# Optimization experiments

Hardware: AMD Instinct MI355X
Metric: run time of the kernel (lower is better)

The kernel has to match this reference:

```python
import jax, jax.numpy as jnp
import numpy as np

B, T, HOR, N = 32, 12, 12, 883
D = 10      # embed_dim == time_dim
HID = 64    # rnn_units
OUT = 1     # output_dim
K = 2       # cheb_k: supports [I, A]


def _pdg2(x, e1, e2, E, Wp, bp):
    # x:[B,N,Ci]  e1,e2:[B,N,D]  E:[N,D]  Wp:[D,K,Ci,Co]  bp:[D,Co]
    nv1 = jnp.tanh(E[None] * e1)                      # [B,N,D]
    nv2 = jnp.tanh(E[None] * e2)
    A = jax.nn.softmax(jax.nn.relu(jnp.einsum('bnd,bmd->bnm', nv1, nv2)), axis=-1)
    xg = jnp.stack([x, jnp.einsum('bnm,bmc->bnc', A, x)], axis=2)   # [B,N,K,Ci]
    W = jnp.einsum('bnd,dkio->bnkio', nv1, Wp)        # node/time-adaptive weights
    b = jnp.einsum('bnd,do->bno', nv1, bp)
    return jnp.einsum('bnki,bnkio->bno', xg, W) + b


def _cell(x, h, e1, e2, E, gW, gb, uW, ub):
    xs = jnp.concatenate([x, h], axis=-1)
    zr = jax.nn.sigmoid(_pdg2(xs, e1, e2, E, gW, gb))
    z, r = jnp.split(zr, 2, axis=-1)
    cand = jnp.concatenate([x, z * h], axis=-1)
    hc = jnp.tanh(_pdg2(cand, e1, e2, E, uW, ub))
    return r * h + (1.0 - r) * hc


def setup_inputs() -> dict:
    key = jax.random.key(0)
    ks = jax.random.split(key, 20)
    s = 0.1
    inp = {
        'src_vals': jax.random.normal(ks[0], (B, T, N, 1), jnp.float32),
        'node_emb': s * jax.random.normal(ks[1], (N, D), jnp.float32),
        'tid_emb1': s * jax.random.normal(ks[2], (288, D), jnp.float32),
        'tid_emb2': s * jax.random.normal(ks[3], (288, D), jnp.float32),
        'diw_emb1': s * jax.random.normal(ks[4], (7, D), jnp.float32),
        'diw_emb2': s * jax.random.normal(ks[5], (7, D), jnp.float32),
        'enc_gate_W': s * jax.random.normal(ks[6], (D, K, 1 + HID, 2 * HID), jnp.float32),
        'enc_gate_b': s * jax.random.normal(ks[7], (D, 2 * HID), jnp.float32),
        'enc_upd_W': s * jax.random.normal(ks[8], (D, K, 1 + HID, HID), jnp.float32),
        'enc_upd_b': s * jax.random.normal(ks[9], (D, HID), jnp.float32),
        'dec_gate_W': s * jax.random.normal(ks[10], (D, K, OUT + HID, 2 * HID), jnp.float32),
        'dec_gate_b': s * jax.random.normal(ks[11], (D, 2 * HID), jnp.float32),
        'dec_upd_W': s * jax.random.normal(ks[12], (D, K, OUT + HID, HID), jnp.float32),
        'dec_upd_b': s * jax.random.normal(ks[13], (D, HID), jnp.float32),
        'proj_W': s * jax.random.normal(ks[14], (OUT, HID), jnp.float32),
        'proj_b': jnp.zeros((OUT,), jnp.float32),
        'src_tid': jax.random.randint(ks[15], (B, T, N), 0, 288, jnp.int32),
        'src_diw': jax.random.randint(ks[16], (B, T, N), 0, 7, jnp.int32),
        'tgt_tid': jax.random.randint(ks[17], (B, HOR, N), 0, 288, jnp.int32),
        'tgt_diw': jax.random.randint(ks[18], (B, HOR, N), 0, 7, jnp.int32),
    }
    return inp


def reference(src_vals, node_emb, tid_emb1, tid_emb2, diw_emb1, diw_emb2,
              enc_gate_W, enc_gate_b, enc_upd_W, enc_upd_b,
              dec_gate_W, dec_gate_b, dec_upd_W, dec_upd_b,
              proj_W, proj_b, src_tid, src_diw, tgt_tid, tgt_diw):
    tm = lambda a: jnp.swapaxes(a, 0, 1)   # batch-major -> time-major
    # periodic embeddings (use_week=True -> elementwise product)
    e1_en = tid_emb1[src_tid] * diw_emb1[src_diw]   # [B,T,N,D]
    e2_en = tid_emb2[src_tid] * diw_emb2[src_diw]
    e1_de = tid_emb1[tgt_tid] * diw_emb1[tgt_diw]   # [B,HOR,N,D]
    e2_de = tid_emb2[tgt_tid] * diw_emb2[tgt_diw]

    h0 = jnp.zeros((src_vals.shape[0], node_emb.shape[0], HID), src_vals.dtype)

    def enc_step(h, inp):
        x, e1, e2 = inp
        h = _cell(x, h, e1, e2, node_emb, enc_gate_W, enc_gate_b, enc_upd_W, enc_upd_b)
        return h, None

    h, _ = jax.lax.scan(enc_step, h0, (tm(src_vals), tm(e1_en), tm(e2_en)))

    go0 = jnp.zeros((src_vals.shape[0], node_emb.shape[0], OUT), src_vals.dtype)

    def dec_step(carry, inp):
        h, go = carry
        e1, e2 = inp
        h = _cell(go, h, e1, e2, node_emb, dec_gate_W, dec_gate_b, dec_upd_W, dec_upd_b)
        go = h @ proj_W.T + proj_b
        return (h, go), go

    _, outs = jax.lax.scan(dec_step, (h, go0), (tm(e1_de), tm(e2_de)))
    return jnp.swapaxes(outs, 0, 1)   # [B,HOR,N,OUT]
```

## Files before the change

### kernel.cpp

```cpp
#include <hip/hip_runtime.h>

#define BB 32
#define TSRC 12
#define HORZ 12
#define NN 883
#define DD 10
#define HH 64
#define BN (BB*NN)
#define BNP 28288
#define KF 5
#define NT 14
#define NST (TSRC+HORZ)

typedef __attribute__((ext_vector_type(8))) short short8;
typedef __attribute__((ext_vector_type(4))) float f32x4;

static __device__ __forceinline__ float sigmf(float x) { return 1.f/(1.f + __expf(-x)); }
static __device__ __forceinline__ float tanh_fast(float x) {
  float e = __expf(2.f*x);
  return (e - 1.f) / (e + 1.f);
}
static __device__ __forceinline__ unsigned int bf_hi(float f) {
  unsigned int u = __float_as_uint(f);
  return (u + 0x7fffu + ((u >> 16) & 1u)) >> 16;
}
static __device__ __forceinline__ float bf_f(unsigned int h) {
  return __uint_as_float(h << 16);
}
static __device__ __forceinline__ void lds_load16(const void* g, void* l) {
  __builtin_amdgcn_global_load_lds(
      (const __attribute__((address_space(1))) void*)g,
      (__attribute__((address_space(3))) void*)l, 16, 0, 0);
}

static __device__ __forceinline__ void swz_block(int& b, int& rt) {
  int lin = blockIdx.x + blockIdx.y*NT;
  int c = lin & 7, q = lin >> 3;
  b = c + ((q/NT) << 3);
  rt = q - (q/NT)*NT;
}

static __device__ __forceinline__ void xs_store(unsigned short* chunk, int c, int mm2, float v) {
  int p0 = (c*128 + (mm2 ^ ((c & 7) << 4))) >> 1;
  unsigned int hi = bf_hi(v);
  chunk[p0] = (unsigned short)hi;
  chunk[p0 + 4096] = (unsigned short)bf_hi(v - bf_f(hi));
}

__global__ __launch_bounds__(256) void prep_all(
    const float* __restrict__ tidE1, const float* __restrict__ tidE2,
    const float* __restrict__ diwE1, const float* __restrict__ diwE2,
    const float* __restrict__ nodeE,
    const int* __restrict__ stid, const int* __restrict__ sdiw,
    const int* __restrict__ ttid, const int* __restrict__ tdiw,
    const float* __restrict__ xsrc,
    float* __restrict__ nv1A, float* __restrict__ nv2A,
    unsigned short* __restrict__ XsH, unsigned short* __restrict__ XsZ)
{
  int i = blockIdx.x*256 + threadIdx.x;
  if (i >= BN) return;
  int st = blockIdx.y;
  int b = i / NN, n = i - b*NN;
  const int* tix = (st < TSRC) ? stid : ttid;
  const int* dix = (st < TSRC) ? sdiw : tdiw;
  int t = (st < TSRC) ? st : st - TSRC;
  int gi = (b*TSRC + t)*NN + n;
  int ti = tix[gi]*DD, di = dix[gi]*DD;
  int nE = n*DD;
  float* nv1T = nv1A + (size_t)st*DD*BNP;
  float* nv2T = nv2A + (size_t)st*DD*BNP;
#pragma unroll
  for (int d = 0; d < DD; ++d) {
    float E = nodeE[nE+d];
    nv1T[d*BNP+i] = tanh_fast(E * (tidE1[ti+d] * diwE1[di+d]));
    nv2T[d*BNP+i] = tanh_fast(E * (tidE2[ti+d] * diwE2[di+d]));
  }
  if (st == 0) {
    float xv = xsrc[gi];
    size_t cb = ((size_t)(b*NT + (n >> 6)))*8192;
    int mm = n & 63;
    unsigned int hi = bf_hi(xv);
    unsigned short los = (unsigned short)bf_hi(xv - bf_f(hi));
    XsH[cb + mm] = (unsigned short)hi; XsH[cb + 4096 + mm] = los;
    XsZ[cb + mm] = (unsigned short)hi; XsZ[cb + 4096 + mm] = los;
  }
}

__global__ __launch_bounds__(256) void wsplit_kernel(
    const float* __restrict__ W, const float* __restrict__ bias,
    int NO, unsigned short* __restrict__ Wf)
{
  int i = blockIdx.x*256 + threadIdx.x;
  int total = DD*2*KF*4*NO*8;
  if (i >= total) return;
  int j = i & 7; int r = i >> 3;
  int o = r % NO; r /= NO;
  int quad = r & 3; r >>= 2;
  int kf = r % KF; r /= KF;
  int hl = r & 1; int d = r >> 1;
  int kk = kf*32 + quad*8 + j;
  float v = 0.f;
  if (kk <= 64)       v = W[(size_t)(d*130 + kk)*NO + o];
  else if (kk == 65)  v = bias[d*NO + o];
  else if (kk <= 130) v = W[(size_t)(d*130 + kk - 1)*NO + o];
  unsigned int hi = bf_hi(v);
  Wf[i] = (hl == 0) ? (unsigned short)hi : (unsigned short)bf_hi(v - bf_f(hi));
}


__global__ __launch_bounds__(256,3) void attn_gate(
    const float* __restrict__ nv1T, const float* __restrict__ nv2T,
    const unsigned short* __restrict__ Xs,
    const float* __restrict__ h,
    const unsigned short* __restrict__ Wf,
    float* __restrict__ rbuf,
    unsigned short* __restrict__ XsZ, float* __restrict__ zh63)
{
  __shared__ float nv1s[DD][64];
  __shared__ float linv[64];
  __shared__ alignas(16) unsigned char U[46080];
  unsigned short* XT = (unsigned short*)U;
  unsigned short* PT = (unsigned short*)(U + 16384);
  float* nv2s = (float*)(U + 34816);
  float* xcolb = (float*)(U + 39936);
  int b, rt;
  swz_block(b, rt);
  int r0 = rt*64;
  int tid = threadIdx.x;
  int rg = tid >> 4, cg = tid & 15;
  int base = b*NN;
  int lane = tid & 63, lm = lane & 15, quad = lane >> 4;
  int w = tid >> 6, mp = w >> 1, np = w & 1;
  const unsigned short* XsB = Xs + (size_t)b*NT*8192;

  for (int idx = tid; idx < DD*64; idx += 256) {
    int d = idx >> 6, r = idx & 63;
    nv1s[d][r] = (r0 + r < NN) ? nv1T[d*BNP + base + r0 + r] : 0.f;
  }

  int4 xt[4];
  float nvr[3]; float xcr;
  {
    const int4* s0 = (const int4*)XsB;
#pragma unroll
    for (int i = 0; i < 4; ++i) xt[i] = s0[w*64 + lane + i*256];
#pragma unroll
    for (int i = 0; i < 3; ++i) {
      int idx = tid + i*256; float v = 0.f;
      if (idx < DD*64) { int d = idx>>6, m = idx&63; v = (m < NN) ? nv2T[d*BNP + base + m] : 0.f; }
      nvr[i] = v;
    }
    xcr = (tid < 64 && tid < NN) ? h[(size_t)63*BNP + base + tid] : 0.f;
#pragma unroll
    for (int i = 0; i < 4; ++i)
      *(int4*)((char*)XT + w*1024 + lane*16 + i*4096) = xt[i];
#pragma unroll
    for (int i = 0; i < 3; ++i) {
      int idx = tid + i*256;
      if (idx < DD*64) nv2s[idx] = nvr[i];
    }
    if (tid < 64) xcolb[tid] = xcr;
  }
  __syncthreads();

  f32x4 accv[2][2] = {};
  float acclp[4] = {}, acc5p[4] = {};

  for (int tI = 0; tI < NT; ++tI) {
    int cur = tI & 1, nxt = cur ^ 1;
    int m0 = tI*64, m0n = m0 + 64;
    bool hasn = tI < NT-1;
    if (hasn) {
      const int4* src = (const int4*)(XsB + (size_t)(tI+1)*8192);
#pragma unroll
      for (int i = 0; i < 4; ++i) xt[i] = src[w*64 + lane + i*256];
#pragma unroll
      for (int i = 0; i < 3; ++i) {
        int idx = tid + i*256; float v = 0.f;
        if (idx < DD*64) { int d = idx>>6, m = idx&63; v = (m0n + m < NN) ? nv2T[d*BNP + base + m0n + m] : 0.f; }
        nvr[i] = v;
      }
      xcr = (tid < 64 && m0n + tid < NN) ? h[(size_t)63*BNP + base + m0n + tid] : 0.f;
    }
    float s[4][4] = {};
#pragma unroll
    for (int d = 0; d < DD; ++d) {
      float4 a4 = *(const float4*)&nv1s[d][rg*4];
      float4 c4 = *(const float4*)&nv2s[cur*(DD*64) + d*64 + cg*4];
      const float* ap = (const float*)&a4;
      const float* cp = (const float*)&c4;
#pragma unroll
      for (int j = 0; j < 4; ++j)
#pragma unroll
        for (int jj = 0; jj < 4; ++jj)
          s[j][jj] += ap[j]*cp[jj];
    }
    int mvlim = NN - m0;
    float ev[4][4];
#pragma unroll
    for (int jj = 0; jj < 4; ++jj) {
      int m = cg*4 + jj;
      float xm = xcolb[cur*64 + m];
      bool okm = m < mvlim;
#pragma unroll
      for (int j = 0; j < 4; ++j) {
        float e = okm ? __expf(fmaxf(s[j][jj], 0.f)) : 0.f;
        ev[j][jj] = e;
        acclp[j] += e;
        acc5p[j] = fmaf(e, xm, acc5p[j]);
      }
    }
    {
      unsigned int* P1 = (unsigned int*)PT;
      unsigned int* P2 = (unsigned int*)(PT + 64*72);
#pragma unroll
      for (int j = 0; j < 4; ++j) {
        int r = rg*4 + j;
        unsigned int h0 = bf_hi(ev[j][0]), h1 = bf_hi(ev[j][1]), h2 = bf_hi(ev[j][2]), h3 = bf_hi(ev[j][3]);
        unsigned int l0 = bf_hi(ev[j][0]-bf_f(h0)), l1 = bf_hi(ev[j][1]-bf_f(h1));
        unsigned int l2 = bf_hi(ev[j][2]-bf_f(h2)), l3 = bf_hi(ev[j][3]-bf_f(h3));
        int dw = r*36 + cg*2;
        P1[dw] = h0 | (h1 << 16); P1[dw+1] = h2 | (h3 << 16);
        P2[dw] = l0 | (l1 << 16); P2[dw+1] = l2 | (l3 << 16);
      }
    }
    __syncthreads();
    {
      short8 Aa[2][2], Ab[2][2], Ba[2][2], Bb[2][2];
#pragma unroll
      for (int mt = 0; mt < 2; ++mt) {
        int r = mp*32 + mt*16 + lm;
#pragma unroll
        for (int kf = 0; kf < 2; ++kf) {
          Aa[mt][kf] = *(const short8*)&PT[r*72 + quad*8 + kf*32];
          Ab[mt][kf] = *(const short8*)&PT[64*72 + r*72 + quad*8 + kf*32];
        }
      }
#pragma unroll
      for (int ntl = 0; ntl < 2; ++ntl) {
        int c = np*32 + ntl*16 + lm;
        int swz = (c & 7) << 4;
        int cb0 = c*128 + quad*16;
#pragma unroll
        for (int kf = 0; kf < 2; ++kf) {
          int a = (cb0 + kf*64) ^ swz;
          Ba[ntl][kf] = *(const short8*)((const char*)XT + a);
          Bb[ntl][kf] = *(const short8*)((const char*)XT + a + 8192);
        }
      }
#pragma unroll
      for (int kf = 0; kf < 2; ++kf)
#pragma unroll
        for (int mt = 0; mt < 2; ++mt)
#pragma unroll
          for (int ntl = 0; ntl < 2; ++ntl) {
            accv[mt][ntl] = __builtin_amdgcn_mfma_f32_16x16x32_bf16(Aa[mt][kf], Ba[ntl][kf], accv[mt][ntl], 0,0,0);
            accv[mt][ntl] = __builtin_amdgcn_mfma_f32_16x16x32_bf16(Aa[mt][kf], Bb[ntl][kf], accv[mt][ntl], 0,0,0);
            accv[mt][ntl] = __builtin_amdgcn_mfma_f32_16x16x32_bf16(Ab[mt][kf], Ba[ntl][kf], accv[mt][ntl], 0,0,0);
          }
    }
    if (hasn) {
#pragma unroll
      for (int i = 0; i < 3; ++i) {
        int idx = tid + i*256;
        if (idx < DD*64) nv2s[nxt*(DD*64) + idx] = nvr[i];
      }
      if (tid < 64) xcolb[nxt*64 + tid] = xcr;
    }
    __syncthreads();
    if (hasn) {
#pragma unroll
      for (int i = 0; i < 4; ++i)
        *(int4*)((char*)XT + w*1024 + lane*16 + i*4096) = xt[i];
    }
  }
  int mrow_x = tid >> 2, ksub = tid & 3;
  int gmx = base + r0 + mrow_x;
  const unsigned short* chk_in = Xs + (size_t)(b*NT + rt)*8192;
  int mm2x = mrow_x*2;
  unsigned int pjh[9], pjl[9];
  {
    float r63v = h[(size_t)63*BNP + gmx];
    unsigned int h63 = bf_hi(r63v);
    unsigned int l63 = bf_hi(r63v - bf_f(h63));
#pragma unroll
    for (int i = 0; i < 9; ++i) {
      int kk = ksub*2 + 8*i;
      unsigned int h0 = 0, l0 = 0, h1 = 0, l1 = 0;
      if (kk <= 63) {
        int idx = (kk*128 + (mm2x ^ ((kk & 7) << 4))) >> 1;
        h0 = chk_in[idx]; l0 = chk_in[idx + 4096];
      } else if (kk == 64) { h0 = h63; l0 = l63; }
      int k1 = kk + 1;
      if (kk <= 62) {
        int idx1 = (k1*128 + (mm2x ^ ((k1 & 7) << 4))) >> 1;
        h1 = chk_in[idx1]; l1 = chk_in[idx1 + 4096];
      } else if (k1 == 65) { h1 = 0x3F80u; l1 = 0u; }
      pjh[i] = h0 | (h1 << 16);
      pjl[i] = l0 | (l1 << 16);
    }
  }
#pragma unroll
  for (int off = 1; off <= 8; off <<= 1)
#pragma unroll
    for (int j = 0; j < 4; ++j) {
      acclp[j] += __shfl_xor(acclp[j], off, 64);
      acc5p[j] += __shfl_xor(acc5p[j], off, 64);
    }
  __syncthreads();
  {
    unsigned int* Z = (unsigned int*)(U + 36864);
    for (int idx = tid; idx < 2304; idx += 256) Z[idx] = 0;
  }
  __syncthreads();
  unsigned short* XA = (unsigned short*)U;
  if (cg == 0) {
#pragma unroll
    for (int j = 0; j < 4; ++j) {
      float li = 1.f / acclp[j];
      int r = rg*4 + j;
      linv[r] = li;
      float v = acc5p[j]*li;
      unsigned int hi = bf_hi(v);
      XA[(4*64 + r)*72 + 2] = (unsigned short)hi;
      XA[(4*64 + r)*72 + 32 + 2] = (unsigned short)bf_hi(v - bf_f(hi));
    }
  }
  __syncthreads();
#pragma unroll
  for (int mt = 0; mt < 2; ++mt) {
    int rbase = mp*32 + mt*16 + quad*4;
    float4 lv = *(const float4*)&linv[rbase];
    const float* lvp = (const float*)&lv;
#pragma unroll
    for (int ntl = 0; ntl < 2; ++ntl) {
      int c = np*32 + ntl*16 + lm;
      int kk = 66 + c;
      int kf = kk >> 5, kkl = kk & 31;
#pragma unroll
      for (int r4 = 0; r4 < 4; ++r4) {
        float v = accv[mt][ntl][r4] * lvp[r4];
        unsigned int hi = bf_hi(v);
        int p = (kf*64 + rbase + r4)*72 + kkl;
        XA[p] = (unsigned short)hi;
        XA[p + 32] = (unsigned short)bf_hi(v - bf_f(hi));
      }
    }
  }
  {
    unsigned int* X1 = (unsigned int*)U;
#pragma unroll
    for (int i = 0; i < 9; ++i) {
      int kk = ksub*2 + 8*i;
      if (kk > 64) continue;
      int kf = kk >> 5, kkl = kk & 31;
      int dw = (kf*64 + mrow_x)*36 + (kkl >> 1);
      X1[dw] = pjh[i];
      X1[dw + 16] = pjl[i];
    }
  }
  __syncthreads();
  short8 A1[2][KF], A2[2][KF];
#pragma unroll
  for (int mt = 0; mt < 2; ++mt) {
    int mrow = mp*32 + mt*16 + lm;
#pragma unroll
    for (int kf = 0; kf < KF; ++kf) {
      A1[mt][kf] = *(const short8*)&XA[(kf*64 + mrow)*72 + quad*8];
      A2[mt][kf] = *(const short8*)&XA[(kf*64 + mrow)*72 + 32 + quad*8];
    }
  }
  __syncthreads();
  unsigned char* bufA = U;
  unsigned char* bufB = U + 20480;
  const int colb = np*32 + lm;
#pragma unroll 1
  for (int co = 0; co < 2; ++co) {
    int co0 = co*64;
    {
      const unsigned short* src = Wf + ((size_t)(w*5)*128 + co0)*8 + lane*8;
#pragma unroll
      for (int i = 0; i < 5; ++i)
        lds_load16(src + (size_t)i*128*8, bufA + (w*5+i)*1024);
    }
    f32x4 accO[2][2] = {};
#pragma unroll 1
    for (int d = 0; d < DD; ++d) {
      f32x4 td[2][2] = {};
      __syncthreads();
      {
        const unsigned short* src = Wf + ((size_t)((d*2+1)*20 + w*5)*128 + co0)*8 + lane*8;
#pragma unroll
        for (int i = 0; i < 5; ++i)
          lds_load16(src + (size_t)i*128*8, bufB + (w*5+i)*1024);
      }
#pragma unroll
      for (int kf = 0; kf < KF; ++kf) {
        int cb = ((kf*4 + quad)*64 + colb)*16;
#pragma unroll
        for (int ntl = 0; ntl < 2; ++ntl) {
          short8 Bh = *(const short8*)(bufA + cb + ntl*256);
          td[0][ntl] = __builtin_amdgcn_mfma_f32_16x16x32_bf16(A1[0][kf], Bh, td[0][ntl], 0,0,0);
          td[0][ntl] = __builtin_amdgcn_mfma_f32_16x16x32_bf16(A2[0][kf], Bh, td[0][ntl], 0,0,0);
          td[1][ntl] = __builtin_amdgcn_mfma_f32_16x16x32_bf16(A1[1][kf], Bh, td[1][ntl], 0,0,0);
          td[1][ntl] = __builtin_amdgcn_mfma_f32_16x16x32_bf16(A2[1][kf], Bh, td[1][ntl], 0,0,0);
        }
      }
      __syncthreads();
      if (d < DD-1) {
        const unsigned short* src = Wf + ((size_t)((d+1)*2*20 + w*5)*128 + co0)*8 + lane*8;
#pragma unroll
        for (int i = 0; i < 5; ++i)
          lds_load16(src + (size_t)i*128*8, bufA + (w*5+i)*1024);
      }
#pragma unroll
      for (int kf = 0; kf < KF; ++kf) {
        int cb = ((kf*4 + quad)*64 + colb)*16;
#pragma unroll
        for (int ntl = 0; ntl < 2; ++ntl) {
          short8 Bl = *(const short8*)(bufB + cb + ntl*256);
          td[0][ntl] = __builtin_amdgcn_mfma_f32_16x16x32_bf16(A1[0][kf], Bl, td[0][ntl], 0,0,0);
          td[1][ntl] = __builtin_amdgcn_mfma_f32_16x16x32_bf16(A1[1][kf], Bl, td[1][ntl], 0,0,0);
        }
      }
#pragma unroll
      for (int mt = 0; mt < 2; ++mt) {
        float4 nv4 = *(const float4*)&nv1s[d][mp*32 + mt*16 + quad*4];
        const float* nvp = (const float*)&nv4;
#pragma unroll
        for (int ntl = 0; ntl < 2; ++ntl)
#pragma unroll
          for (int r = 0; r < 4; ++r)
            accO[mt][ntl][r] += nvp[r] * td[mt][ntl][r];
      }
    }
    float* CT = (float*)U;
    __syncthreads();
#pragma unroll
    for (int mt = 0; mt < 2; ++mt)
#pragma unroll
      for (int ntl = 0; ntl < 2; ++ntl)
#pragma unroll
        for (int r = 0; r < 4; ++r)
          CT[(mp*32 + mt*16 + quad*4 + r)*67 + np*32 + ntl*16 + lm] = accO[mt][ntl][r];
    __syncthreads();
    {
      int mm = tid & 63, og = tid >> 6;
      int n = r0 + mm;
      int gm = base + n;
      bool okn = n < NN;
      if (co == 0) {
        unsigned short* chk = XsZ + ((size_t)(b*NT + rt))*8192;
        int mm2 = mm*2;
        for (int j = 0; j < 16; ++j) {
          int o = og*16 + j;
          float z = sigmf(CT[mm*67 + o]);
          float zhv = z * h[(size_t)o*BNP + gm];
          if (okn) {
            if (o < 63) xs_store(chk, o + 1, mm2, zhv);
            else zh63[gm] = zhv;
          }
        }
      } else {
        for (int j = 0; j < 16; ++j) {
          int o = og*16 + j;
          if (okn) rbuf[(size_t)o*BNP + gm] = sigmf(CT[mm*67 + o]);
        }
      }
    }
    __syncthreads();
  }
}

__global__ __launch_bounds__(256,3) void attn_upd(
    const float* __restrict__ nv1T, const float* __restrict__ nv2T,
    const unsigned short* __restrict__ Xs,
    const float* __restrict__ zh63,
    float* __restrict__ hstate,
    const unsigned short* __restrict__ Wf,
    const float* __restrict__ rbuf,
    int dec, const float* __restrict__ pW, const float* __restrict__ pb,
    float* __restrict__ go, float* __restrict__ dout,
    unsigned short* __restrict__ XsH, int t,
    const float* __restrict__ xsrc, int xnmode, int xnt,
    unsigned short* __restrict__ XsZm)
{
  __shared__ float nv1s[DD][64];
  __shared__ float linv[64];
  __shared__ alignas(16) unsigned char U[46080];
  unsigned short* XT = (unsigned short*)U;
  unsigned short* PT = (unsigned short*)(U + 16384);
  float* nv2s = (float*)(U + 34816);
  float* xcolb = (float*)(U + 39936);
  int b, rt;
  swz_block(b, rt);
  int r0 = rt*64;
  int tid = threadIdx.x;
  int rg = tid >> 4, cg = tid & 15;
  int base = b*NN;
  int lane = tid & 63, lm = lane & 15, quad = lane >> 4;
  int w = tid >> 6, mp = w >> 1, np = w & 1;
  const unsigned short* XsB = Xs + (size_t)b*NT*8192;

  for (int idx = tid; idx < DD*64; idx += 256) {
    int d = idx >> 6, r = idx & 63;
    nv1s[d][r] = (r0 + r < NN) ? nv1T[d*BNP + base + r0 + r] : 0.f;
  }

  int4 xt[4];
  float nvr[3]; float xcr;
  {
    const int4* s0 = (const int4*)XsB;
#pragma unroll
    for (int i = 0; i < 4; ++i) xt[i] = s0[w*64 + lane + i*256];
#pragma unroll
    for (int i = 0; i < 3; ++i) {
      int idx = tid + i*256; float v = 0.f;
      if (idx < DD*64) { int d = idx>>6, m = idx&63; v = (m < NN) ? nv2T[d*BNP + base + m] : 0.f; }
      nvr[i] = v;
    }
    xcr = (tid < 64 && tid < NN) ? zh63[base + tid] : 0.f;
#pragma unroll
    for (int i = 0; i < 4; ++i)
      *(int4*)((char*)XT + w*1024 + lane*16 + i*4096) = xt[i];
#pragma unroll
    for (int i = 0; i < 3; ++i) {
      int idx = tid + i*256;
      if (idx < DD*64) nv2s[idx] = nvr[i];
    }
    if (tid < 64) xcolb[tid] = xcr;
  }
  __syncthreads();

  f32x4 accv[2][2] = {};
  float acclp[4] = {}, acc5p[4] = {};

  for (int tI = 0; tI < NT; ++tI) {
    int cur = tI & 1, nxt = cur ^ 1;
    int m0 = tI*64, m0n = m0 + 64;
    bool hasn = tI < NT-1;
    if (hasn) {
      const int4* src = (const int4*)(XsB + (size_t)(tI+1)*8192);
#pragma unroll
      for (int i = 0; i < 4; ++i) xt[i] = src[w*64 + lane + i*256];
#pragma unroll
      for (int i = 0; i < 3; ++i) {
        int idx = tid + i*256; float v = 0.f;
        if (idx < DD*64) { int d = idx>>6, m = idx&63; v = (m0n + m < NN) ? nv2T[d*BNP + base + m0n + m] : 0.f; }
        nvr[i] = v;
      }
      xcr = (tid < 64 && m0n + tid < NN) ? zh63[base + m0n + tid] : 0.f;
    }
    float s[4][4] = {};
#pragma unroll
    for (int d = 0; d < DD; ++d) {
      float4 a4 = *(const float4*)&nv1s[d][rg*4];
      float4 c4 = *(const float4*)&nv2s[cur*(DD*64) + d*64 + cg*4];
      const float* ap = (const float*)&a4;
      const float* cp = (const float*)&c4;
#pragma unroll
      for (int j = 0; j < 4; ++j)
#pragma unroll
        for (int jj = 0; jj < 4; ++jj)
          s[j][jj] += ap[j]*cp[jj];
    }
    int mvlim = NN - m0;
    float ev[4][4];
#pragma unroll
    for (int jj = 0; jj < 4; ++jj) {
      int m = cg*4 + jj;
      float xm = xcolb[cur*64 + m];
      bool okm = m < mvlim;
#pragma unroll
      for (int j = 0; j < 4; ++j) {
        float e = okm ? __expf(fmaxf(s[j][jj], 0.f)) : 0.f;
        ev[j][jj] = e;
        acclp[j] += e;
        acc5p[j] = fmaf(e, xm, acc5p[j]);
      }
    }
    {
      unsigned int* P1 = (unsigned int*)PT;
      unsigned int* P2 = (unsigned int*)(PT + 64*72);
#pragma unroll
      for (int j = 0; j < 4; ++j) {
        int r = rg*4 + j;
        unsigned int h0 = bf_hi(ev[j][0]), h1 = bf_hi(ev[j][1]), h2 = bf_hi(ev[j][2]), h3 = bf_hi(ev[j][3]);
        unsigned int l0 = bf_hi(ev[j][0]-bf_f(h0)), l1 = bf_hi(ev[j][1]-bf_f(h1));
        unsigned int l2 = bf_hi(ev[j][2]-bf_f(h2)), l3 = bf_hi(ev[j][3]-bf_f(h3));
        int dw = r*36 + cg*2;
        P1[dw] = h0 | (h1 << 16); P1[dw+1] = h2 | (h3 << 16);
        P2[dw] = l0 | (l1 << 16); P2[dw+1] = l2 | (l3 << 16);
      }
    }
    __syncthreads();
    {
      short8 Aa[2][2], Ab[2][2], Ba[2][2], Bb[2][2];
#pragma unroll
      for (int mt = 0; mt < 2; ++mt) {
        int r = mp*32 + mt*16 + lm;
#pragma unroll
        for (int kf = 0; kf < 2; ++kf) {
          Aa[mt][kf] = *(const short8*)&PT[r*72 + quad*8 + kf*32];
          Ab[mt][kf] = *(const short8*)&PT[64*72 + r*72 + quad*8 + kf*32];
        }
      }
#pragma unroll
      for (int ntl = 0; ntl < 2; ++ntl) {
        int c = np*32 + ntl*16 + lm;
        int swz = (c & 7) << 4;
        int cb0 = c*128 + quad*16;
#pragma unroll
        for (int kf = 0; kf < 2; ++kf) {
          int a = (cb0 + kf*64) ^ swz;
          Ba[ntl][kf] = *(const short8*)((const char*)XT + a);
          Bb[ntl][kf] = *(const short8*)((const char*)XT + a + 8192);
        }
      }
#pragma unroll
      for (int kf = 0; kf < 2; ++kf)
#pragma unroll
        for (int mt = 0; mt < 2; ++mt)
#pragma unroll
          for (int ntl = 0; ntl < 2; ++ntl) {
            accv[mt][ntl] = __builtin_amdgcn_mfma_f32_16x16x32_bf16(Aa[mt][kf], Ba[ntl][kf], accv[mt][ntl], 0,0,0);
            accv[mt][ntl] = __builtin_amdgcn_mfma_f32_16x16x32_bf16(Aa[mt][kf], Bb[ntl][kf], accv[mt][ntl], 0,0,0);
            accv[mt][ntl] = __builtin_amdgcn_mfma_f32_16x16x32_bf16(Ab[mt][kf], Ba[ntl][kf], accv[mt][ntl], 0,0,0);
          }
    }
    if (hasn) {
#pragma unroll
      for (int i = 0; i < 3; ++i) {
        int idx = tid + i*256;
        if (idx < DD*64) nv2s[nxt*(DD*64) + idx] = nvr[i];
      }
      if (tid < 64) xcolb[nxt*64 + tid] = xcr;
    }
    __syncthreads();
    if (hasn) {
#pragma unroll
      for (int i = 0; i < 4; ++i)
        *(int4*)((char*)XT + w*1024 + lane*16 + i*4096) = xt[i];
    }
  }
  int mrow_x = tid >> 2, ksub = tid & 3;
  int gmx = base + r0 + mrow_x;
  const unsigned short* chk_in = Xs + (size_t)(b*NT + rt)*8192;
  int mm2x = mrow_x*2;
  unsigned int pjh[9], pjl[9];
  {
    float r63v = zh63[gmx];
    unsigned int h63 = bf_hi(r63v);
    unsigned int l63 = bf_hi(r63v - bf_f(h63));
#pragma unroll
    for (int i = 0; i < 9; ++i) {
      int kk = ksub*2 + 8*i;
      unsigned int h0 = 0, l0 = 0, h1 = 0, l1 = 0;
      if (kk <= 63) {
        int idx = (kk*128 + (mm2x ^ ((kk & 7) << 4))) >> 1;
        h0 = chk_in[idx]; l0 = chk_in[idx + 4096];
      } else if (kk == 64) { h0 = h63; l0 = l63; }
      int k1 = kk + 1;
      if (kk <= 62) {
        int idx1 = (k1*128 + (mm2x ^ ((k1 & 7) << 4))) >> 1;
        h1 = chk_in[idx1]; l1 = chk_in[idx1 + 4096];
      } else if (k1 == 65) { h1 = 0x3F80u; l1 = 0u; }
      pjh[i] = h0 | (h1 << 16);
      pjl[i] = l0 | (l1 << 16);
    }
  }
#pragma unroll
  for (int off = 1; off <= 8; off <<= 1)
#pragma unroll
    for (int j = 0; j < 4; ++j) {
      acclp[j] += __shfl_xor(acclp[j], off, 64);
      acc5p[j] += __shfl_xor(acc5p[j], off, 64);
    }
  __syncthreads();
  {
    unsigned int* Z = (unsigned int*)(U + 36864);
    for (int idx = tid; idx < 2304; idx += 256) Z[idx] = 0;
  }
  __syncthreads();
  unsigned short* XA = (unsigned short*)U;
  if (cg == 0) {
#pragma unroll
    for (int j = 0; j < 4; ++j) {
      float li = 1.f / acclp[j];
      int r = rg*4 + j;
      linv[r] = li;
      float v = acc5p[j]*li;
      unsigned int hi = bf_hi(v);
      XA[(4*64 + r)*72 + 2] = (unsigned short)hi;
      XA[(4*64 + r)*72 + 32 + 2] = (unsigned short)bf_hi(v - bf_f(hi));
    }
  }
  __syncthreads();
#pragma unroll
  for (int mt = 0; mt < 2; ++mt) {
    int rbase = mp*32 + mt*16 + quad*4;
    float4 lv = *(const float4*)&linv[rbase];
    const float* lvp = (const float*)&lv;
#pragma unroll
    for (int ntl = 0; ntl < 2; ++ntl) {
      int c = np*32 + ntl*16 + lm;
      int kk = 66 + c;
      int kf = kk >> 5, kkl = kk & 31;
#pragma unroll
      for (int r4 = 0; r4 < 4; ++r4) {
        float v = accv[mt][ntl][r4] * lvp[r4];
        unsigned int hi = bf_hi(v);
        int p = (kf*64 + rbase + r4)*72 + kkl;
        XA[p] = (unsigned short)hi;
        XA[p + 32] = (unsigned short)bf_hi(v - bf_f(hi));
      }
    }
  }
  {
    unsigned int* X1 = (unsigned int*)U;
#pragma unroll
    for (int i = 0; i < 9; ++i) {
      int kk = ksub*2 + 8*i;
      if (kk > 64) continue;
      int kf = kk >> 5, kkl = kk & 31;
      int dw = (kf*64 + mrow_x)*36 + (kkl >> 1);
      X1[dw] = pjh[i];
      X1[dw + 16] = pjl[i];
    }
  }
  __syncthreads();
  short8 A1[2][KF], A2[2][KF];
#pragma unroll
  for (int mt = 0; mt < 2; ++mt) {
    int mrow = mp*32 + mt*16 + lm;
#pragma unroll
    for (int kf = 0; kf < KF; ++kf) {
      A1[mt][kf] = *(const short8*)&XA[(kf*64 + mrow)*72 + quad*8];
      A2[mt][kf] = *(const short8*)&XA[(kf*64 + mrow)*72 + 32 + quad*8];
    }
  }
  __syncthreads();
  unsigned char* bufA = U;
  unsigned char* bufB = U + 20480;
  const int colb = np*32 + lm;
  {
    const unsigned short* src = Wf + (size_t)(w*5)*64*8 + lane*8;
#pragma unroll
    for (int i = 0; i < 5; ++i)
      lds_load16(src + (size_t)i*64*8, bufA + (w*5+i)*1024);
  }
  f32x4 accO[2][2] = {};
#pragma unroll 1
  for (int d = 0; d < DD; ++d) {
    f32x4 td[2][2] = {};
    __syncthreads();
    {
      const unsigned short* src = Wf + (size_t)((d*2+1)*20 + w*5)*64*8 + lane*8;
#pragma unroll
      for (int i = 0; i < 5; ++i)
        lds_load16(src + (size_t)i*64*8, bufB + (w*5+i)*1024);
    }
#pragma unroll
    for (int kf = 0; kf < KF; ++kf) {
      int cb = ((kf*4 + quad)*64 + colb)*16;
#pragma unroll
      for (int ntl = 0; ntl < 2; ++ntl) {
        short8 Bh = *(const short8*)(bufA + cb + ntl*256);
        td[0][ntl] = __builtin_amdgcn_mfma_f32_16x16x32_bf16(A1[0][kf], Bh, td[0][ntl], 0,0,0);
        td[0][ntl] = __builtin_amdgcn_mfma_f32_16x16x32_bf16(A2[0][kf], Bh, td[0][ntl], 0,0,0);
        td[1][ntl] = __builtin_amdgcn_mfma_f32_16x16x32_bf16(A1[1][kf], Bh, td[1][ntl], 0,0,0);
        td[1][ntl] = __builtin_amdgcn_mfma_f32_16x16x32_bf16(A2[1][kf], Bh, td[1][ntl], 0,0,0);
      }
    }
    __syncthreads();
    if (d < DD-1) {
      const unsigned short* src = Wf + (size_t)((d+1)*2*20 + w*5)*64*8 + lane*8;
#pragma unroll
      for (int i = 0; i < 5; ++i)
        lds_load16(src + (size_t)i*64*8, bufA + (w*5+i)*1024);
    }
#pragma unroll
    for (int kf = 0; kf < KF; ++kf) {
      int cb = ((kf*4 + quad)*64 + colb)*16;
#pragma unroll
      for (int ntl = 0; ntl < 2; ++ntl) {
        short8 Bl = *(const short8*)(bufB + cb + ntl*256);
        td[0][ntl] = __builtin_amdgcn_mfma_f32_16x16x32_bf16(A1[0][kf], Bl, td[0][ntl], 0,0,0);
        td[1][ntl] = __builtin_amdgcn_mfma_f32_16x16x32_bf16(A1[1][kf], Bl, td[1][ntl], 0,0,0);
      }
    }
#pragma unroll
    for (int mt = 0; mt < 2; ++mt) {
      float4 nv4 = *(const float4*)&nv1s[d][mp*32 + mt*16 + quad*4];
      const float* nvp = (const float*)&nv4;
#pragma unroll
      for (int ntl = 0; ntl < 2; ++ntl)
#pragma unroll
        for (int r = 0; r < 4; ++r)
          accO[mt][ntl][r] += nvp[r] * td[mt][ntl][r];
    }
  }
  float* CT = (float*)U;
  __syncthreads();
#pragma unroll
  for (int mt = 0; mt < 2; ++mt)
#pragma unroll
    for (int ntl = 0; ntl < 2; ++ntl)
#pragma unroll
      for (int r = 0; r < 4; ++r)
        CT[(mp*32 + mt*16 + quad*4 + r)*67 + np*32 + ntl*16 + lm] = accO[mt][ntl][r];
  __syncthreads();
  {
    int mm = tid & 63, og = tid >> 6;
    int n = r0 + mm;
    int gm = base + n;
    bool okn = n < NN;
    unsigned short* chk = XsH + ((size_t)(b*NT + rt))*8192;
    int mm2 = mm*2;
    float pp = 0.f;
    float sval = 0.f;
    for (int j = 0; j < 16; ++j) {
      int o = og*16 + j;
      float hc = tanhf(CT[mm*67 + o]);
      float r = rbuf[(size_t)o*BNP + gm];
      float hv = hstate[(size_t)o*BNP + gm];
      float hn = r*hv + (1.f - r)*hc;
      if (okn) {
        hstate[(size_t)o*BNP + gm] = hn;
        if (o < 63) xs_store(chk, o + 1, mm2, hn);
      }
      if (dec) pp = fmaf(hn, pW[o], pp);
    }
    if (dec) {
      float* PS = CT + 64*67;
      __syncthreads();
      PS[mm*4 + og] = pp;
      __syncthreads();
      if (tid < 64) {
        int n2 = r0 + tid;
        if (n2 < NN) {
          float s = pb[0] + PS[tid*4] + PS[tid*4+1] + PS[tid*4+2] + PS[tid*4+3];
          go[base + n2] = s;
          dout[(b*HORZ + t)*NN + n2] = s;
          sval = s;
        }
      }
    }
    if (xnmode) {
      if (tid < 64) {
        int n2 = r0 + tid;
        if (n2 < NN) {
          float xn;
          if (xnmode == 1)      xn = xsrc[(b*TSRC + xnt)*NN + n2];
          else if (xnmode == 2) xn = 0.f;
          else                  xn = sval;
          unsigned int hix = bf_hi(xn);
          unsigned short lox = (unsigned short)bf_hi(xn - bf_f(hix));
          unsigned short* cH = XsH + ((size_t)(b*NT + rt))*8192;
          unsigned short* cZ = XsZm + ((size_t)(b*NT + rt))*8192;
          cH[tid] = (unsigned short)hix; cH[4096 + tid] = lox;
          cZ[tid] = (unsigned short)hix; cZ[4096 + tid] = lox;
        }
      }
    }
  }
}

extern "C" void kernel_launch(void* const* d_in, const int* in_sizes, int n_in,
                              void* d_out, int out_size, void* d_ws, size_t ws_size,
                              hipStream_t stream) {
  (void)in_sizes; (void)n_in; (void)out_size; (void)ws_size;
  const float* src_vals = (const float*)d_in[0];
  const float* node_emb = (const float*)d_in[1];
  const float* tid1 = (const float*)d_in[2];
  const float* tid2 = (const float*)d_in[3];
  const float* diw1 = (const float*)d_in[4];
  const float* diw2 = (const float*)d_in[5];
  const float* egW = (const float*)d_in[6];
  const float* egb = (const float*)d_in[7];
  const float* euW = (const float*)d_in[8];
  const float* eub = (const float*)d_in[9];
  const float* dgW = (const float*)d_in[10];
  const float* dgb = (const float*)d_in[11];
  const float* duW = (const float*)d_in[12];
  const float* dub = (const float*)d_in[13];
  const float* pW  = (const float*)d_in[14];
  const float* pb  = (const float*)d_in[15];
  const int* stid = (const int*)d_in[16];
  const int* sdiw = (const int*)d_in[17];
  const int* ttid = (const int*)d_in[18];
  const int* tdiw = (const int*)d_in[19];
  float* out = (float*)d_out;

  float* wp = (float*)d_ws;
  float* hbuf = wp; wp += (size_t)64*BNP;
  float* zh63 = wp; wp += BNP + 64;
  float* rbuf = wp; wp += (size_t)64*BNP;
  float* nv1A = wp; wp += (size_t)NST*DD*BNP;
  float* nv2A = wp; wp += (size_t)NST*DD*BNP;
  float* go   = wp; wp += BN + 64;
  unsigned short* egS = (unsigned short*)wp; wp += 204800;
  unsigned short* dgS = (unsigned short*)wp; wp += 204800;
  unsigned short* euS = (unsigned short*)wp; wp += 102400;
  unsigned short* duS = (unsigned short*)wp; wp += 102400;
  unsigned short* XsH = (unsigned short*)wp; wp += 1835008;
  unsigned short* XsZ = (unsigned short*)wp; wp += 1835008;

  hipMemsetAsync(hbuf, 0, sizeof(float)*(size_t)64*BNP, stream);
  hipMemsetAsync(go, 0, sizeof(float)*(BN+64), stream);
  hipMemsetAsync(XsH, 0, (size_t)BB*NT*16384, stream);
  hipMemsetAsync(XsZ, 0, (size_t)BB*NT*16384, stream);

  wsplit_kernel<<<1600,256,0,stream>>>(egW, egb, 128, egS);
  wsplit_kernel<<<1600,256,0,stream>>>(dgW, dgb, 128, dgS);
  wsplit_kernel<<<800,256,0,stream>>>(euW, eub, 64, euS);
  wsplit_kernel<<<800,256,0,stream>>>(duW, dub, 64, duS);

  dim3 pgrid(111, NST);
  prep_all<<<pgrid,256,0,stream>>>(tid1,tid2,diw1,diw2,node_emb,stid,sdiw,ttid,tdiw,src_vals,nv1A,nv2A,XsH,XsZ);

  dim3 fgrid(NT, BB);
  for (int t = 0; t < TSRC; ++t) {
    const float* n1 = nv1A + (size_t)t*DD*BNP;
    const float* n2 = nv2A + (size_t)t*DD*BNP;
    attn_gate<<<fgrid,256,0,stream>>>(n1,n2,XsH,hbuf,egS,rbuf,XsZ,zh63);
    int xnm = (t < TSRC-1) ? 1 : 2;
    attn_upd<<<fgrid,256,0,stream>>>(n1,n2,XsZ,zh63,hbuf,euS,rbuf,0,pW,pb,go,out,XsH,t,src_vals,xnm,t+1,XsZ);
  }
  for (int t = 0; t < HORZ; ++t) {
    const float* n1 = nv1A + (size_t)(TSRC+t)*DD*BNP;
    const float* n2 = nv2A + (size_t)(TSRC+t)*DD*BNP;
    attn_gate<<<fgrid,256,0,stream>>>(n1,n2,XsH,hbuf,dgS,rbuf,XsZ,zh63);
    int xnm = (t < HORZ-1) ? 3 : 0;
    attn_upd<<<fgrid,256,0,stream>>>(n1,n2,XsZ,zh63,hbuf,duS,rbuf,1,pW,pb,go,out,XsH,t,src_vals,xnm,0,XsZ);
  }
}
```

Baseline: 4.376 ms.

## Triple-buffer weight tiles in LDS with partial vmcnt waits

```diff
diff --git a/kernel.cpp b/kernel.cpp
--- a/kernel.cpp
+++ b/kernel.cpp
@@ -32,6 +32,8 @@
       (const __attribute__((address_space(1))) void*)g,
       (__attribute__((address_space(3))) void*)l, 16, 0, 0);
 }
+#define WB5() asm volatile("s_waitcnt vmcnt(5)\n\ts_barrier" ::: "memory")
+#define WB0() asm volatile("s_waitcnt vmcnt(0)\n\ts_barrier" ::: "memory")
 
 static __device__ __forceinline__ void swz_block(int& b, int& rt) {
   int lin = blockIdx.x + blockIdx.y*NT;
@@ -108,7 +110,7 @@
 }
 
 
-__global__ __launch_bounds__(256,3) void attn_gate(
+__global__ __launch_bounds__(256,2) void attn_gate(
     const float* __restrict__ nv1T, const float* __restrict__ nv2T,
     const unsigned short* __restrict__ Xs,
     const float* __restrict__ h,
@@ -118,7 +120,7 @@
 {
   __shared__ float nv1s[DD][64];
   __shared__ float linv[64];
-  __shared__ alignas(16) unsigned char U[46080];
+  __shared__ alignas(16) unsigned char U[61440];
   unsigned short* XT = (unsigned short*)U;
   unsigned short* PT = (unsigned short*)(U + 16384);
   float* nv2s = (float*)(U + 34816);
@@ -371,54 +373,59 @@
     }
   }
   __syncthreads();
-  unsigned char* bufA = U;
-  unsigned char* bufB = U + 20480;
   const int colb = np*32 + lm;
 #pragma unroll 1
   for (int co = 0; co < 2; ++co) {
     int co0 = co*64;
     {
-      const unsigned short* src = Wf + ((size_t)(w*5)*128 + co0)*8 + lane*8;
-#pragma unroll
-      for (int i = 0; i < 5; ++i)
-        lds_load16(src + (size_t)i*128*8, bufA + (w*5+i)*1024);
+      const unsigned short* sA = Wf + ((size_t)(0*20 + w*5)*128 + co0)*8 + lane*8;
+      const unsigned short* sB = Wf + ((size_t)(1*20 + w*5)*128 + co0)*8 + lane*8;
+#pragma unroll
+      for (int i = 0; i < 5; ++i) lds_load16(sA + (size_t)i*128*8, U + (w*5+i)*1024);
+#pragma unroll
+      for (int i = 0; i < 5; ++i) lds_load16(sB + (size_t)i*128*8, U + 20480 + (w*5+i)*1024);
     }
     f32x4 accO[2][2] = {};
 #pragma unroll 1
     for (int d = 0; d < DD; ++d) {
       f32x4 td[2][2] = {};
-      __syncthreads();
-      {
-        const unsigned short* src = Wf + ((size_t)((d*2+1)*20 + w*5)*128 + co0)*8 + lane*8;
-#pragma unroll
-        for (int i = 0; i < 5; ++i)
-          lds_load16(src + (size_t)i*128*8, bufB + (w*5+i)*1024);
+      int s0i = 2*d;
+      unsigned char* Bh_buf = U + (s0i % 3)*20480;
+      unsigned char* Bl_buf = U + ((s0i+1) % 3)*20480;
+      WB5();
+      if (d < DD-1) {
+        int sn = s0i + 2;
+        unsigned char* bn = U + (sn % 3)*20480;
+        const unsigned short* src = Wf + ((size_t)(sn*20 + w*5)*128 + co0)*8 + lane*8;
+#pragma unroll
+        for (int i = 0; i < 5; ++i) lds_load16(src + (size_t)i*128*8, bn + (w*5+i)*1024);
       }
 #pragma unroll
       for (int kf = 0; kf < KF; ++kf) {
         int cb = ((kf*4 + quad)*64 + colb)*16;
 #pragma unroll
         for (int ntl = 0; ntl < 2; ++ntl) {
-          short8 Bh = *(const short8*)(bufA + cb + ntl*256);
+          short8 Bh = *(const short8*)(Bh_buf + cb + ntl*256);
           td[0][ntl] = __builtin_amdgcn_mfma_f32_16x16x32_bf16(A1[0][kf], Bh, td[0][ntl], 0,0,0);
           td[0][ntl] = __builtin_amdgcn_mfma_f32_16x16x32_bf16(A2[0][kf], Bh, td[0][ntl], 0,0,0);
           td[1][ntl] = __builtin_amdgcn_mfma_f32_16x16x32_bf16(A1[1][kf], Bh, td[1][ntl], 0,0,0);
           td[1][ntl] = __builtin_amdgcn_mfma_f32_16x16x32_bf16(A2[1][kf], Bh, td[1][ntl], 0,0,0);
         }
       }
-      __syncthreads();
+      if (d < DD-1) WB5(); else WB0();
       if (d < DD-1) {
-        const unsigned short* src = Wf + ((size_t)((d+1)*2*20 + w*5)*128 + co0)*8 + lane*8;
-#pragma unroll
-        for (int i = 0; i < 5; ++i)
-          lds_load16(src + (size_t)i*128*8, bufA + (w*5+i)*1024);
+        int sn = s0i + 3;
+        unsigned char* bn = U + (sn % 3)*20480;
+        const unsigned short* src = Wf + ((size_t)(sn*20 + w*5)*128 + co0)*8 + lane*8;
+#pragma unroll
+        for (int i = 0; i < 5; ++i) lds_load16(src + (size_t)i*128*8, bn + (w*5+i)*1024);
       }
 #pragma unroll
       for (int kf = 0; kf < KF; ++kf) {
         int cb = ((kf*4 + quad)*64 + colb)*16;
 #pragma unroll
         for (int ntl = 0; ntl < 2; ++ntl) {
-          short8 Bl = *(const short8*)(bufB + cb + ntl*256);
+          short8 Bl = *(const short8*)(Bl_buf + cb + ntl*256);
           td[0][ntl] = __builtin_amdgcn_mfma_f32_16x16x32_bf16(A1[0][kf], Bl, td[0][ntl], 0,0,0);
           td[1][ntl] = __builtin_amdgcn_mfma_f32_16x16x32_bf16(A1[1][kf], Bl, td[1][ntl], 0,0,0);
         }
@@ -472,7 +479,7 @@
   }
 }
 
-__global__ __launch_bounds__(256,3) void attn_upd(
+__global__ __launch_bounds__(256,2) void attn_upd(
     const float* __restrict__ nv1T, const float* __restrict__ nv2T,
     const unsigned short* __restrict__ Xs,
     const float* __restrict__ zh63,
@@ -487,7 +494,7 @@
 {
   __shared__ float nv1s[DD][64];
   __shared__ float linv[64];
-  __shared__ alignas(16) unsigned char U[46080];
+  __shared__ alignas(16) unsigned char U[61440];
   unsigned short* XT = (unsigned short*)U;
   unsigned short* PT = (unsigned short*)(U + 16384);
   float* nv2s = (float*)(U + 34816);
@@ -740,51 +747,56 @@
     }
   }
   __syncthreads();
-  unsigned char* bufA = U;
-  unsigned char* bufB = U + 20480;
   const int colb = np*32 + lm;
   {
-    const unsigned short* src = Wf + (size_t)(w*5)*64*8 + lane*8;
-#pragma unroll
-    for (int i = 0; i < 5; ++i)
-      lds_load16(src + (size_t)i*64*8, bufA + (w*5+i)*1024);
+    const unsigned short* sA = Wf + (size_t)(0*20 + w*5)*64*8 + lane*8;
+    const unsigned short* sB = Wf + (size_t)(1*20 + w*5)*64*8 + lane*8;
+#pragma unroll
+    for (int i = 0; i < 5; ++i) lds_load16(sA + (size_t)i*64*8, U + (w*5+i)*1024);
+#pragma unroll
+    for (int i = 0; i < 5; ++i) lds_load16(sB + (size_t)i*64*8, U + 20480 + (w*5+i)*1024);
   }
   f32x4 accO[2][2] = {};
 #pragma unroll 1
   for (int d = 0; d < DD; ++d) {
     f32x4 td[2][2] = {};
-    __syncthreads();
-    {
-      const unsigned short* src = Wf + (size_t)((d*2+1)*20 + w*5)*64*8 + lane*8;
-#pragma unroll
-      for (int i = 0; i < 5; ++i)
-        lds_load16(src + (size_t)i*64*8, bufB + (w*5+i)*1024);
+    int s0i = 2*d;
+    unsigned char* Bh_buf = U + (s0i % 3)*20480;
+    unsigned char* Bl_buf = U + ((s0i+1) % 3)*20480;
+    WB5();
+    if (d < DD-1) {
+      int sn = s0i + 2;
+      unsigned char* bn = U + (sn % 3)*20480;
+      const unsigned short* src = Wf + (size_t)(sn*20 + w*5)*64*8 + lane*8;
+#pragma unroll
+      for (int i = 0; i < 5; ++i) lds_load16(src + (size_t)i*64*8, bn + (w*5+i)*1024);
     }
 #pragma unroll
     for (int kf = 0; kf < KF; ++kf) {
       int cb = ((kf*4 + quad)*64 + colb)*16;
 #pragma unroll
       for (int ntl = 0; ntl < 2; ++ntl) {
-        short8 Bh = *(const short8*)(bufA + cb + ntl*256);
+        short8 Bh = *(const short8*)(Bh_buf + cb + ntl*256);
         td[0][ntl] = __builtin_amdgcn_mfma_f32_16x16x32_bf16(A1[0][kf], Bh, td[0][ntl], 0,0,0);
         td[0][ntl] = __builtin_amdgcn_mfma_f32_16x16x32_bf16(A2[0][kf], Bh, td[0][ntl], 0,0,0);
         td[1][ntl] = __builtin_amdgcn_mfma_f32_16x16x32_bf16(A1[1][kf], Bh, td[1][ntl], 0,0,0);
         td[1][ntl] = __builtin_amdgcn_mfma_f32_16x16x32_bf16(A2[1][kf], Bh, td[1][ntl], 0,0,0);
       }
     }
-    __syncthreads();
+    if (d < DD-1) WB5(); else WB0();
     if (d < DD-1) {
-      const unsigned short* src = Wf + (size_t)((d+1)*2*20 + w*5)*64*8 + lane*8;
-#pragma unroll
-      for (int i = 0; i < 5; ++i)
-        lds_load16(src + (size_t)i*64*8, bufA + (w*5+i)*1024);
+      int sn = s0i + 3;
+      unsigned char* bn = U + (sn % 3)*20480;
+      const unsigned short* src = Wf + (size_t)(sn*20 + w*5)*64*8 + lane*8;
+#pragma unroll
+      for (int i = 0; i < 5; ++i) lds_load16(src + (size_t)i*64*8, bn + (w*5+i)*1024);
     }
 #pragma unroll
     for (int kf = 0; kf < KF; ++kf) {
       int cb = ((kf*4 + quad)*64 + colb)*16;
 #pragma unroll
       for (int ntl = 0; ntl < 2; ++ntl) {
-        short8 Bl = *(const short8*)(bufB + cb + ntl*256);
+        short8 Bl = *(const short8*)(Bl_buf + cb + ntl*256);
         td[0][ntl] = __builtin_amdgcn_mfma_f32_16x16x32_bf16(A1[0][kf], Bl, td[0][ntl], 0,0,0);
         td[1][ntl] = __builtin_amdgcn_mfma_f32_16x16x32_bf16(A1[1][kf], Bl, td[1][ntl], 0,0,0);
       }
```

New measurement: 4.658 ms. +6.4%, slower.
